# Kernel tuning notes

Hardware: AMD Instinct MI355X
Metric: run time of the kernel (lower is better)

The kernel has to match this reference:

```python
import jax, jax.numpy as jnp
import numpy as np

PATCH_SIZE = 16  # init_kwargs patch_size


def setup_inputs() -> dict:
    key = jax.random.key(0)
    k1, k2, k3 = jax.random.split(key, 3)
    B, C, H, W = 128, 3, 224, 224
    n_points = int(H * W * 0.5 / PATCH_SIZE ** 2)  # 98
    imgs = jax.random.normal(k1, (B, C, H, W), dtype=jnp.float32)
    points_x = jax.random.randint(k2, (B, n_points), 0, H - PATCH_SIZE + 1, dtype=jnp.int32)
    points_y = jax.random.randint(k3, (B, n_points), 0, W - PATCH_SIZE + 1, dtype=jnp.int32)
    return {"imgs": imgs, "points_x": points_x, "points_y": points_y}


def reference(imgs, points_x, points_y):
    # imgs: [B, C, H, W]; points_x/points_y: [B, N] top-left corners of P x P patches to zero.
    B, C, H, W = imgs.shape
    P = PATCH_SIZE
    off = jnp.arange(P, dtype=points_x.dtype)
    b = jnp.arange(B)[:, None, None, None]                       # [B,1,1,1]
    xs = points_x[:, :, None, None] + off[None, None, :, None]    # [B,N,P,1]
    ys = points_y[:, :, None, None] + off[None, None, None, :]    # [B,N,1,P]
    # Build occlusion mask once with a single scatter, then apply across channels.
    mask = jnp.zeros((B, H, W), dtype=jnp.bool_).at[b, xs, ys].set(True)  # [B,H,W]
    return jnp.where(mask[:, None, :, :], jnp.zeros((), imgs.dtype), imgs)
```

## Files before the change

### kernel.cpp

```cpp
#include <hip/hip_runtime.h>

#define BB 128
#define CC 3
#define HH 224
#define WW 224
#define PP 16

#define W4 (WW / 4)
#define CHAN4 (HH * W4)
#define PER_IMG4 (CC * CHAN4)
#define NROWS 6
#define NBLK (BB * (CHAN4 / 256))

typedef float vfloat4 __attribute__((ext_vector_type(4)));

__global__ __launch_bounds__(256) void occl_fused(
        vfloat4* __restrict__ out, const vfloat4* __restrict__ imgs,
        const int* __restrict__ px, const int* __restrict__ py, int N) {
    const int t     = threadIdx.x;
    const int b     = blockIdx.x / (CHAN4 / 256);
    const int posF0 = (blockIdx.x % (CHAN4 / 256)) * 256;
    const int h0    = posF0 / W4;

    __shared__ unsigned int rowbits[NROWS * 7];
    if (t < NROWS * 7) rowbits[t] = 0u;
    __syncthreads();

    if (t < N) {
        int x = px[b * N + t];
        int y = py[b * N + t];
        int lo = x > h0 ? x : h0;
        int hi = (x + PP < h0 + NROWS) ? (x + PP) : (h0 + NROWS);
        if (lo < hi) {
            unsigned long long mm = 0xFFFFull << (y & 31);
            unsigned int lo32 = (unsigned int)mm;
            unsigned int hi32 = (unsigned int)(mm >> 32);
            int woff = y >> 5;
            for (int h = lo; h < hi; ++h) {
                int base = (h - h0) * 7 + woff;
                atomicOr(&rowbits[base], lo32);
                if (hi32) atomicOr(&rowbits[base + 1], hi32);
            }
        }
    }
    __syncthreads();

    int p  = posF0 + t;
    int w4 = p % W4;
    int h  = p / W4;
    unsigned int word = rowbits[(h - h0) * 7 + (w4 >> 3)];
    unsigned int m4 = (word >> ((w4 & 7) * 4)) & 0xFu;

    size_t f0 = (size_t)b * PER_IMG4 + p;
    vfloat4 z = {0.f, 0.f, 0.f, 0.f};
    vfloat4 v0 = z, v1 = z, v2 = z;
    if (m4 != 0xFu) {
        v0 = __builtin_nontemporal_load(&imgs[f0]);
        v1 = __builtin_nontemporal_load(&imgs[f0 + CHAN4]);
        v2 = __builtin_nontemporal_load(&imgs[f0 + 2 * CHAN4]);
        if (m4 & 1u) { v0.x = 0.f; v1.x = 0.f; v2.x = 0.f; }
        if (m4 & 2u) { v0.y = 0.f; v1.y = 0.f; v2.y = 0.f; }
        if (m4 & 4u) { v0.z = 0.f; v1.z = 0.f; v2.z = 0.f; }
        if (m4 & 8u) { v0.w = 0.f; v1.w = 0.f; v2.w = 0.f; }
    }
    __builtin_nontemporal_store(v0, &out[f0]);
    __builtin_nontemporal_store(v1, &out[f0 + CHAN4]);
    __builtin_nontemporal_store(v2, &out[f0 + 2 * CHAN4]);
}

extern "C" void kernel_launch(void* const* d_in, const int* in_sizes, int n_in,
                              void* d_out, int out_size, void* d_ws, size_t ws_size,
                              hipStream_t stream) {
    const float* imgs = (const float*)d_in[0];
    const int*   px   = (const int*)d_in[1];
    const int*   py   = (const int*)d_in[2];
    float*       out  = (float*)d_out;

    const int N = in_sizes[1] / BB;

    occl_fused<<<NBLK, 256, 0, stream>>>(
        (vfloat4*)out, (const vfloat4*)imgs, px, py, N);
}
```

Baseline: 136.0 us.

## Split mask construction into a separate per-image kernel using workspace bitmasks

```diff
diff --git a/kernel.cpp b/kernel.cpp
--- a/kernel.cpp
+++ b/kernel.cpp
@@ -9,11 +9,73 @@
 #define W4 (WW / 4)
 #define CHAN4 (HH * W4)
 #define PER_IMG4 (CC * CHAN4)
-#define NROWS 6
 #define NBLK (BB * (CHAN4 / 256))
+
+#define MROW 8
+#define MIMG (HH * MROW)
+#define MASK_BYTES ((size_t)BB * MIMG * 4)
 
 typedef float vfloat4 __attribute__((ext_vector_type(4)));
 
+__global__ __launch_bounds__(256) void build_masks(
+        unsigned int* __restrict__ masks, const int* __restrict__ px,
+        const int* __restrict__ py, int N) {
+    const int b = blockIdx.x;
+    const int t = threadIdx.x;
+
+    __shared__ unsigned int rb[MIMG];
+    __shared__ int sx[128], sy[128];
+
+    for (int i = t; i < MIMG; i += 256) rb[i] = 0u;
+    if (t < N) { sx[t] = px[b * N + t]; sy[t] = py[b * N + t]; }
+    __syncthreads();
+
+    for (int idx = t; idx < N * PP; idx += 256) {
+        const int pt = idx >> 4;
+        const int r  = idx & (PP - 1);
+        const int x  = sx[pt] + r;
+        const int y  = sy[pt];
+        unsigned long long mm = 0xFFFFull << (y & 31);
+        const int w = y >> 5;
+        atomicOr(&rb[x * MROW + w], (unsigned int)mm);
+        const unsigned int hi = (unsigned int)(mm >> 32);
+        if (hi) atomicOr(&rb[x * MROW + w + 1], hi);
+    }
+    __syncthreads();
+
+    for (int i = t; i < MIMG; i += 256) masks[b * MIMG + i] = rb[i];
+}
+
+__global__ __launch_bounds__(256) void occl_apply(
+        vfloat4* __restrict__ out, const vfloat4* __restrict__ imgs,
+        const unsigned int* __restrict__ masks) {
+    const int t = threadIdx.x;
+    const int b = blockIdx.x / (CHAN4 / 256);
+    const int p = (blockIdx.x % (CHAN4 / 256)) * 256 + t;
+    const int w4 = p % W4;
+    const int h  = p / W4;
+
+    const unsigned int word = masks[b * MIMG + h * MROW + (w4 >> 3)];
+    const unsigned int m4 = (word >> ((w4 & 7) * 4)) & 0xFu;
+
+    const size_t f0 = (size_t)b * PER_IMG4 + p;
+    vfloat4 z = {0.f, 0.f, 0.f, 0.f};
+    vfloat4 v0 = z, v1 = z, v2 = z;
+    if (m4 != 0xFu) {
+        v0 = __builtin_nontemporal_load(&imgs[f0]);
+        v1 = __builtin_nontemporal_load(&imgs[f0 + CHAN4]);
+        v2 = __builtin_nontemporal_load(&imgs[f0 + 2 * CHAN4]);
+        if (m4 & 1u) { v0.x = 0.f; v1.x = 0.f; v2.x = 0.f; }
+        if (m4 & 2u) { v0.y = 0.f; v1.y = 0.f; v2.y = 0.f; }
+        if (m4 & 4u) { v0.z = 0.f; v1.z = 0.f; v2.z = 0.f; }
+        if (m4 & 8u) { v0.w = 0.f; v1.w = 0.f; v2.w = 0.f; }
+    }
+    __builtin_nontemporal_store(v0, &out[f0]);
+    __builtin_nontemporal_store(v1, &out[f0 + CHAN4]);
+    __builtin_nontemporal_store(v2, &out[f0 + 2 * CHAN4]);
+}
+
+#define NROWS 6
 __global__ __launch_bounds__(256) void occl_fused(
         vfloat4* __restrict__ out, const vfloat4* __restrict__ imgs,
         const int* __restrict__ px, const int* __restrict__ py, int N) {
@@ -78,6 +140,13 @@
 
     const int N = in_sizes[1] / BB;
 
-    occl_fused<<<NBLK, 256, 0, stream>>>(
-        (vfloat4*)out, (const vfloat4*)imgs, px, py, N);
+    if (ws_size >= MASK_BYTES && d_ws != nullptr) {
+        unsigned int* masks = (unsigned int*)d_ws;
+        build_masks<<<BB, 256, 0, stream>>>(masks, px, py, N);
+        occl_apply<<<NBLK, 256, 0, stream>>>(
+            (vfloat4*)out, (const vfloat4*)imgs, masks);
+    } else {
+        occl_fused<<<NBLK, 256, 0, stream>>>(
+            (vfloat4*)out, (const vfloat4*)imgs, px, py, N);
+    }
 }
```

Result: no change. 137.4 us (+1.0%).
